# Performance work log

Measured on AMD Instinct MI355X. Metric: run time of the kernel, lower is better.

Reference implementation:

```python
import jax, jax.numpy as jnp
import numpy as np

N = 4000000   # number of tiny per-element MLPs
H = 8         # hidden width of each MLP (Linear(1,8) -> ReLU -> Linear(8,1))


def setup_inputs() -> dict:
    key = jax.random.key(0)
    kx, k1, kb1, k2, kb2 = jax.random.split(key, 5)
    x = jax.random.normal(kx, (N, 1), dtype=jnp.float32)
    # PyTorch Linear default init: U(-1/sqrt(fan_in), 1/sqrt(fan_in))
    lim1 = 1.0  # fan_in = 1
    W1 = jax.random.uniform(k1, (N, H), dtype=jnp.float32, minval=-lim1, maxval=lim1)   # Linear(1,8) weight per net, squeezed
    b1 = jax.random.uniform(kb1, (N, H), dtype=jnp.float32, minval=-lim1, maxval=lim1)
    lim2 = 1.0 / np.sqrt(H)  # fan_in = 8
    W2 = jax.random.uniform(k2, (N, H), dtype=jnp.float32, minval=-lim2, maxval=lim2)   # Linear(8,1) weight per net, squeezed
    b2 = jax.random.uniform(kb2, (N, 1), dtype=jnp.float32, minval=-lim2, maxval=lim2)
    return {"x": x, "W1": W1, "b1": b1, "W2": W2, "b2": b2}


def reference(x, W1, b1, W2, b2):
    # y[i] = W2[i] @ relu(W1[i] * x[i] + b1[i]) + b2[i]
    # x: [N,1] broadcasts against W1,b1: [N,H]
    h = jax.nn.relu(x * W1 + b1)                      # [N, H]
    y = jnp.sum(h * W2, axis=-1, keepdims=True) + b2  # [N, 1]
    return y
```

## Files before the change

### kernel.cpp

```cpp
#include <hip/hip_runtime.h>


__global__ __launch_bounds__(256) void tiny_mlp_kernel(
    const float*  __restrict__ x,
    const float4* __restrict__ W1,
    const float4* __restrict__ b1,
    const float4* __restrict__ W2,
    const float*  __restrict__ b2,
    float*        __restrict__ y,
    int n)
{
    const int stride = gridDim.x * blockDim.x;
    for (int i = blockIdx.x * blockDim.x + threadIdx.x; i < n; i += stride) {
        const float xi = x[i];

        const float4 w1a = W1[2 * i];
        const float4 w1b = W1[2 * i + 1];
        const float4 b1a = b1[2 * i];
        const float4 b1b = b1[2 * i + 1];
        const float4 w2a = W2[2 * i];
        const float4 w2b = W2[2 * i + 1];

        const float h0 = fmaxf(fmaf(xi, w1a.x, b1a.x), 0.0f);
        const float h1 = fmaxf(fmaf(xi, w1a.y, b1a.y), 0.0f);
        const float h2 = fmaxf(fmaf(xi, w1a.z, b1a.z), 0.0f);
        const float h3 = fmaxf(fmaf(xi, w1a.w, b1a.w), 0.0f);
        const float h4 = fmaxf(fmaf(xi, w1b.x, b1b.x), 0.0f);
        const float h5 = fmaxf(fmaf(xi, w1b.y, b1b.y), 0.0f);
        const float h6 = fmaxf(fmaf(xi, w1b.z, b1b.z), 0.0f);
        const float h7 = fmaxf(fmaf(xi, w1b.w, b1b.w), 0.0f);

        float acc0 = fmaf(h0, w2a.x, b2[i]);
        acc0 = fmaf(h1, w2a.y, acc0);
        acc0 = fmaf(h2, w2a.z, acc0);
        acc0 = fmaf(h3, w2a.w, acc0);
        float acc1 = h4 * w2b.x;
        acc1 = fmaf(h5, w2b.y, acc1);
        acc1 = fmaf(h6, w2b.z, acc1);
        acc1 = fmaf(h7, w2b.w, acc1);

        y[i] = acc0 + acc1;
    }
}

extern "C" void kernel_launch(void* const* d_in, const int* in_sizes, int n_in,
                              void* d_out, int out_size, void* d_ws, size_t ws_size,
                              hipStream_t stream) {
    const float*  x  = (const float*) d_in[0];
    const float4* W1 = (const float4*)d_in[1];
    const float4* b1 = (const float4*)d_in[2];
    const float4* W2 = (const float4*)d_in[3];
    const float*  b2 = (const float*) d_in[4];
    float*        y  = (float*)d_out;

    const int n = in_sizes[0];

    const int block = 256;
    int grid = (n + block - 1) / block;
    if (grid > 2048) grid = 2048;

    tiny_mlp_kernel<<<grid, block, 0, stream>>>(x, W1, b1, W2, b2, y, n);
}
```

Measured before the change: 368.8 us.

## Split each MLP across two lanes with shuffle reduction and full grid

Each tiny MLP is now handled by two adjacent threads, each loading one float4 from W1, b1 and W2, so consecutive lanes read consecutive 16-byte chunks. The two partial sums are combined with a lane shuffle, and the even lane writes the output. The grid-stride loop is replaced by one thread per half-MLP with a full-size grid. This is meant to improve coalescing and memory-level parallelism in a bandwidth-bound kernel, at the cost of duplicate x loads and idle odd lanes during the store.

```diff
diff --git a/kernel.cpp b/kernel.cpp
--- a/kernel.cpp
+++ b/kernel.cpp
@@ -3,43 +3,36 @@
 
 __global__ __launch_bounds__(256) void tiny_mlp_kernel(
     const float*  __restrict__ x,
-    const float4* __restrict__ W1,
-    const float4* __restrict__ b1,
-    const float4* __restrict__ W2,
+    const float4* __restrict__ W1v,
+    const float4* __restrict__ b1v,
+    const float4* __restrict__ W2v,
     const float*  __restrict__ b2,
     float*        __restrict__ y,
     int n)
 {
-    const int stride = gridDim.x * blockDim.x;
-    for (int i = blockIdx.x * blockDim.x + threadIdx.x; i < n; i += stride) {
-        const float xi = x[i];
+    const int t = blockIdx.x * blockDim.x + threadIdx.x;
+    if (t >= 2 * n) return;
+    const int i = t >> 1;
 
-        const float4 w1a = W1[2 * i];
-        const float4 w1b = W1[2 * i + 1];
-        const float4 b1a = b1[2 * i];
-        const float4 b1b = b1[2 * i + 1];
-        const float4 w2a = W2[2 * i];
-        const float4 w2b = W2[2 * i + 1];
+    const float  xi = x[i];
+    const float4 w1 = W1v[t];
+    const float4 c1 = b1v[t];
+    const float4 w2 = W2v[t];
 
-        const float h0 = fmaxf(fmaf(xi, w1a.x, b1a.x), 0.0f);
-        const float h1 = fmaxf(fmaf(xi, w1a.y, b1a.y), 0.0f);
-        const float h2 = fmaxf(fmaf(xi, w1a.z, b1a.z), 0.0f);
-        const float h3 = fmaxf(fmaf(xi, w1a.w, b1a.w), 0.0f);
-        const float h4 = fmaxf(fmaf(xi, w1b.x, b1b.x), 0.0f);
-        const float h5 = fmaxf(fmaf(xi, w1b.y, b1b.y), 0.0f);
-        const float h6 = fmaxf(fmaf(xi, w1b.z, b1b.z), 0.0f);
-        const float h7 = fmaxf(fmaf(xi, w1b.w, b1b.w), 0.0f);
+    const float h0 = fmaxf(fmaf(xi, w1.x, c1.x), 0.0f);
+    const float h1 = fmaxf(fmaf(xi, w1.y, c1.y), 0.0f);
+    const float h2 = fmaxf(fmaf(xi, w1.z, c1.z), 0.0f);
+    const float h3 = fmaxf(fmaf(xi, w1.w, c1.w), 0.0f);
 
-        float acc0 = fmaf(h0, w2a.x, b2[i]);
-        acc0 = fmaf(h1, w2a.y, acc0);
-        acc0 = fmaf(h2, w2a.z, acc0);
-        acc0 = fmaf(h3, w2a.w, acc0);
-        float acc1 = h4 * w2b.x;
-        acc1 = fmaf(h5, w2b.y, acc1);
-        acc1 = fmaf(h6, w2b.z, acc1);
-        acc1 = fmaf(h7, w2b.w, acc1);
+    float p = h0 * w2.x;
+    p = fmaf(h1, w2.y, p);
+    p = fmaf(h2, w2.z, p);
+    p = fmaf(h3, w2.w, p);
 
-        y[i] = acc0 + acc1;
+    p += __shfl_xor(p, 1);
+
+    if ((t & 1) == 0) {
+        y[i] = p + b2[i];
     }
 }
 
@@ -56,8 +49,8 @@
     const int n = in_sizes[0];
 
     const int block = 256;
-    int grid = (n + block - 1) / block;
-    if (grid > 2048) grid = 2048;
+    const int threads = 2 * n;
+    const int grid = (threads + block - 1) / block;
 
     tiny_mlp_kernel<<<grid, block, 0, stream>>>(x, W1, b1, W2, b2, y, n);
 }
```

Measured after the change: 356.5 us. 1.03x faster.
